# Kernel tuning notes

Hardware: AMD Instinct MI355X
Metric: run time of the kernel (lower is better)

The kernel has to match this reference:

```python
import jax, jax.numpy as jnp
import numpy as np

EPS = 1e-6

def _phi(x):
    # elu_feature_map: elu(x) + 1 (positive feature map)
    return jax.nn.elu(x) + 1.0

def setup_inputs() -> dict:
    key = jax.random.key(0)
    ks = jax.random.split(key, 6)
    N, L, S, H, E, D = 4, 2048, 2048, 16, 64, 64
    return {
        "queries1": jax.random.normal(ks[0], (N, L, H, E), jnp.float32),
        "keys1": jax.random.normal(ks[1], (N, S, H, E), jnp.float32),
        "values1": jax.random.normal(ks[2], (N, S, H, D), jnp.float32),
        "queries2": jax.random.normal(ks[3], (N, L, H, E), jnp.float32),
        "keys2": jax.random.normal(ks[4], (N, S, H, E), jnp.float32),
        "values2": jax.random.normal(ks[5], (N, S, H, D), jnp.float32),
        "key_lengths1": jnp.ones((N, S), jnp.float32),
        "key_lengths2": jnp.ones((N, S), jnp.float32),
    }

def _linear_cross(Q, K_other, V_other):
    # Q: (N,L,H,E) featurized queries; K_other: (N,S,H,E) featurized+masked keys
    # KV: (N,H,D,E) ; 'nshd,nshm->nhmd'
    KV = jnp.einsum('nshd,nshm->nhmd', K_other, V_other)
    Ksum = K_other.sum(axis=1)                      # (N,H,E)
    Z = 1.0 / (jnp.einsum('nlhd,nhd->nlh', Q, Ksum) + EPS)
    # 'nlhd,nhmd,nlh->nlhm'
    return jnp.einsum('nlhd,nhmd->nlhm', Q, KV) * Z[..., None]

def reference(queries1, keys1, values1, queries2, keys2, values2,
              key_lengths1, key_lengths2):
    Q1 = _phi(queries1)
    K1 = _phi(keys1) * key_lengths1[:, :, None, None]
    Q2 = _phi(queries2)
    K2 = _phi(keys2) * key_lengths2[:, :, None, None]
    V1 = _linear_cross(Q1, K2, values2)  # stream1 queries attend to stream2 keys/values
    V2 = _linear_cross(Q2, K1, values1)  # stream2 queries attend to stream1 keys/values
    return (V1, V2)
```

## Files before the change

kernel.cpp:

```cpp
#include <hip/hip_runtime.h>

#define NB 4
#define LL 2048
#define SS 2048
#define HH 16
#define EE 64
#define DD 64

#define KVTOT (2*NB*HH*4096)
#define WSFLOATS (KVTOT + 2*NB*HH*64)

typedef short short8 __attribute__((ext_vector_type(8)));
typedef float floatx4 __attribute__((ext_vector_type(4)));

__device__ inline float phi(float x) { return x > 0.f ? x + 1.f : __expf(x); }

__device__ inline unsigned int f2bf(float f) {
    unsigned int x = __float_as_uint(f);
    return (x + 0x7FFFu + ((x >> 16) & 1u)) >> 16;
}
__device__ inline void split_pack(float a, float b, unsigned int &hp, unsigned int &lp) {
    const unsigned int ha = f2bf(a), hb = f2bf(b);
    const float ra = a - __uint_as_float(ha << 16);
    const float rb = b - __uint_as_float(hb << 16);
    hp = (ha & 0xFFFFu) | (hb << 16);
    lp = (f2bf(ra) & 0xFFFFu) | (f2bf(rb) << 16);
}

__global__ __launch_bounds__(256) void kv_kernel(
    const float* __restrict__ k1, const float* __restrict__ v1,
    const float* __restrict__ k2, const float* __restrict__ v2,
    const float* __restrict__ kl1, const float* __restrict__ kl2,
    float* __restrict__ ws)
{
    const int b = blockIdx.x;
    const int chunk = b & 7;
    const int h = (b >> 3) & 15;
    const int n = (b >> 7) & 3;
    const int st = (b >> 9) & 1;
    const float* K  = st ? k1 : k2;
    const float* V  = st ? v1 : v2;
    const float* KL = st ? kl1 : kl2;

    __shared__ __align__(16) unsigned short KtH[64][72];
    __shared__ __align__(16) unsigned short KtL[64][72];
    __shared__ __align__(16) unsigned short VtH[64][72];
    __shared__ __align__(16) unsigned short VtL[64][72];

    const int t = threadIdx.x;
    const int lane = t & 63;
    const int w = t >> 6;
    const int d4 = t & 15;
    const int sp = t >> 4;
    const int c = lane & 15;
    const int q = lane >> 4;

    float ksum[4] = {0.f, 0.f, 0.f, 0.f};
    floatx4 acc[4];
#pragma unroll
    for (int i = 0; i < 4; i++) acc[i] = (floatx4){0.f, 0.f, 0.f, 0.f};

    float4 cur[8]; float curl[4];
    {
        const int sbase = chunk * 256;
#pragma unroll
        for (int i = 0; i < 2; ++i) {
            const int sl = 2 * sp + 32 * i;
            const size_t off = ((size_t)((size_t)n * SS + sbase + sl) * HH + h) * EE + 4 * d4;
            cur[4 * i + 0] = *(const float4*)&K[off];
            cur[4 * i + 1] = *(const float4*)&K[off + HH * EE];
            cur[4 * i + 2] = *(const float4*)&V[off];
            cur[4 * i + 3] = *(const float4*)&V[off + HH * EE];
            curl[2 * i + 0] = KL[(size_t)n * SS + sbase + sl];
            curl[2 * i + 1] = KL[(size_t)n * SS + sbase + sl + 1];
        }
    }

    for (int g = 0; g < 4; ++g) {
        float4 nxt[8]; float nxtl[4];
        if (g < 3) {
            const int sbase = chunk * 256 + (g + 1) * 64;
#pragma unroll
            for (int i = 0; i < 2; ++i) {
                const int sl = 2 * sp + 32 * i;
                const size_t off = ((size_t)((size_t)n * SS + sbase + sl) * HH + h) * EE + 4 * d4;
                nxt[4 * i + 0] = *(const float4*)&K[off];
                nxt[4 * i + 1] = *(const float4*)&K[off + HH * EE];
                nxt[4 * i + 2] = *(const float4*)&V[off];
                nxt[4 * i + 3] = *(const float4*)&V[off + HH * EE];
                nxtl[2 * i + 0] = KL[(size_t)n * SS + sbase + sl];
                nxtl[2 * i + 1] = KL[(size_t)n * SS + sbase + sl + 1];
            }
        }
        if (g) __syncthreads();
#pragma unroll
        for (int i = 0; i < 2; ++i) {
            const int sl = 2 * sp + 32 * i;
            const float4 ka = cur[4 * i + 0], kb = cur[4 * i + 1];
            const float4 va = cur[4 * i + 2], vb = cur[4 * i + 3];
            const float l0 = curl[2 * i + 0], l1 = curl[2 * i + 1];
            const float a0 = phi(ka.x) * l0, a1 = phi(ka.y) * l0;
            const float a2 = phi(ka.z) * l0, a3 = phi(ka.w) * l0;
            const float b0 = phi(kb.x) * l1, b1 = phi(kb.y) * l1;
            const float b2 = phi(kb.z) * l1, b3 = phi(kb.w) * l1;
            ksum[0] += a0 + b0; ksum[1] += a1 + b1;
            ksum[2] += a2 + b2; ksum[3] += a3 + b3;
            unsigned int hp, lp;
            split_pack(a0, b0, hp, lp);
            *(unsigned int*)&KtH[4 * d4 + 0][sl] = hp; *(unsigned int*)&KtL[4 * d4 + 0][sl] = lp;
            split_pack(a1, b1, hp, lp);
            *(unsigned int*)&KtH[4 * d4 + 1][sl] = hp; *(unsigned int*)&KtL[4 * d4 + 1][sl] = lp;
            split_pack(a2, b2, hp, lp);
            *(unsigned int*)&KtH[4 * d4 + 2][sl] = hp; *(unsigned int*)&KtL[4 * d4 + 2][sl] = lp;
            split_pack(a3, b3, hp, lp);
            *(unsigned int*)&KtH[4 * d4 + 3][sl] = hp; *(unsigned int*)&KtL[4 * d4 + 3][sl] = lp;
            split_pack(va.x, vb.x, hp, lp);
            *(unsigned int*)&VtH[4 * d4 + 0][sl] = hp; *(unsigned int*)&VtL[4 * d4 + 0][sl] = lp;
            split_pack(va.y, vb.y, hp, lp);
            *(unsigned int*)&VtH[4 * d4 + 1][sl] = hp; *(unsigned int*)&VtL[4 * d4 + 1][sl] = lp;
            split_pack(va.z, vb.z, hp, lp);
            *(unsigned int*)&VtH[4 * d4 + 2][sl] = hp; *(unsigned int*)&VtL[4 * d4 + 2][sl] = lp;
            split_pack(va.w, vb.w, hp, lp);
            *(unsigned int*)&VtH[4 * d4 + 3][sl] = hp; *(unsigned int*)&VtL[4 * d4 + 3][sl] = lp;
        }
        __syncthreads();
#pragma unroll
        for (int ks = 0; ks < 2; ++ks) {
            const short8 aH = *(const short8*)&VtH[16 * w + c][32 * ks + 8 * q];
            const short8 aL = *(const short8*)&VtL[16 * w + c][32 * ks + 8 * q];
#pragma unroll
            for (int dt = 0; dt < 4; ++dt) {
                const short8 bH = *(const short8*)&KtH[16 * dt + c][32 * ks + 8 * q];
                const short8 bL = *(const short8*)&KtL[16 * dt + c][32 * ks + 8 * q];
                acc[dt] = __builtin_amdgcn_mfma_f32_16x16x32_bf16(aH, bH, acc[dt], 0, 0, 0);
                acc[dt] = __builtin_amdgcn_mfma_f32_16x16x32_bf16(aH, bL, acc[dt], 0, 0, 0);
                acc[dt] = __builtin_amdgcn_mfma_f32_16x16x32_bf16(aL, bH, acc[dt], 0, 0, 0);
            }
        }
        if (g < 3) {
#pragma unroll
            for (int i = 0; i < 8; ++i) cur[i] = nxt[i];
#pragma unroll
            for (int i = 0; i < 4; ++i) curl[i] = nxtl[i];
        }
    }

    const size_t kvbase = ((size_t)((st * NB + n) * HH + h)) * 4096;
#pragma unroll
    for (int dt = 0; dt < 4; ++dt)
#pragma unroll
        for (int r = 0; r < 4; ++r)
            atomicAdd(&ws[kvbase + (size_t)(16 * w + 4 * q + r) * 64 + 16 * dt + c],
                      acc[dt][r]);

    float (*scr)[64] = (float(*)[64])VtL;
    __syncthreads();
    scr[sp][4 * d4 + 0] = ksum[0];
    scr[sp][4 * d4 + 1] = ksum[1];
    scr[sp][4 * d4 + 2] = ksum[2];
    scr[sp][4 * d4 + 3] = ksum[3];
    __syncthreads();
    if (t < 64) {
        float s = 0.f;
#pragma unroll
        for (int i = 0; i < 16; ++i) s += scr[i][t];
        atomicAdd(&ws[KVTOT + ((size_t)(st * NB + n) * HH + h) * 64 + t], s);
    }
}

static __device__ __forceinline__ float lt_body(
    const float4 qa0, const float4 qb0, const float4 qa1, const float4 qb1,
    const float* Ksp,
    const unsigned short (*BH)[72], const unsigned short (*BL)[72],
    const int c, const int q, floatx4* acc)
{
    float z = 0.f;
#pragma unroll
    for (int ks = 0; ks < 2; ++ks) {
        const float4 qa = ks ? qa1 : qa0;
        const float4 qb = ks ? qb1 : qb0;
        const int co = 32 * ks + 8 * q;
        const float p[8] = {phi(qa.x), phi(qa.y), phi(qa.z), phi(qa.w),
                            phi(qb.x), phi(qb.y), phi(qb.z), phi(qb.w)};
        z += p[0] * Ksp[co + 0] + p[1] * Ksp[co + 1]
           + p[2] * Ksp[co + 2] + p[3] * Ksp[co + 3]
           + p[4] * Ksp[co + 4] + p[5] * Ksp[co + 5]
           + p[6] * Ksp[co + 6] + p[7] * Ksp[co + 7];
        short8 aH, aL;
#pragma unroll
        for (int j = 0; j < 8; ++j) {
            const unsigned int hb = f2bf(p[j]);
            aH[j] = (short)hb;
            aL[j] = (short)f2bf(p[j] - __uint_as_float(hb << 16));
        }
#pragma unroll
        for (int mt = 0; mt < 4; ++mt) {
            const short8 bH = *(const short8*)&BH[16 * mt + c][co];
            const short8 bL = *(const short8*)&BL[16 * mt + c][co];
            acc[mt] = __builtin_amdgcn_mfma_f32_16x16x32_bf16(aH, bH, acc[mt], 0, 0, 0);
            acc[mt] = __builtin_amdgcn_mfma_f32_16x16x32_bf16(aH, bL, acc[mt], 0, 0, 0);
            acc[mt] = __builtin_amdgcn_mfma_f32_16x16x32_bf16(aL, bH, acc[mt], 0, 0, 0);
        }
    }
    return z;
}

__global__ __launch_bounds__(256) void out_kernel(
    const float* __restrict__ q1, const float* __restrict__ q2,
    const float* __restrict__ ws, float* __restrict__ out)
{
    const int b = blockIdx.x;
    const int lc = b & 15;
    const int h = (b >> 4) & 15;
    const int n = (b >> 8) & 3;
    const int st = (b >> 10) & 1;
    const float* Q = st ? q2 : q1;
    float* O = out + (size_t)st * ((size_t)NB * LL * HH * DD);

    __shared__ __align__(16) unsigned short BtH[64][72];
    __shared__ __align__(16) unsigned short BtL[64][72];
    __shared__ float Ks[64];

    const int t = threadIdx.x;
    const int lane = t & 63;
    const int w = t >> 6;
    const int c = lane & 15;
    const int q = lane >> 4;
    const size_t kvbase = ((size_t)((st * NB + n) * HH + h)) * 4096;
    const int lbase = lc * 128;

    const float* qr0 = &Q[((size_t)((size_t)n * LL + lbase + 32 * w + c) * HH + h) * EE];
    const int d0q = 8 * q;
    const float4 p00 = *(const float4*)&qr0[d0q];
    const float4 p01 = *(const float4*)&qr0[d0q + 4];
    const float4 p02 = *(const float4*)&qr0[d0q + 32];
    const float4 p03 = *(const float4*)&qr0[d0q + 36];

    {
        const int m = t >> 2;
        const int dbase = (t & 3) * 16;
#pragma unroll
        for (int i = 0; i < 4; ++i) {
            const int d0 = dbase + 4 * i;
            const float4 kv = *(const float4*)&ws[kvbase + (size_t)m * 64 + d0];
            unsigned int hp, lp;
            split_pack(kv.x, kv.y, hp, lp);
            *(unsigned int*)&BtH[m][d0]     = hp; *(unsigned int*)&BtL[m][d0]     = lp;
            split_pack(kv.z, kv.w, hp, lp);
            *(unsigned int*)&BtH[m][d0 + 2] = hp; *(unsigned int*)&BtL[m][d0 + 2] = lp;
        }
    }
    if (t < 64) Ks[t] = ws[KVTOT + ((size_t)(st * NB + n) * HH + h) * 64 + t];
    __syncthreads();

    floatx4 acc[8];
#pragma unroll
    for (int i = 0; i < 8; ++i) acc[i] = (floatx4){0.f, 0.f, 0.f, 0.f};

    float z0 = lt_body(p00, p01, p02, p03, Ks, BtH, BtL, c, q, acc);

    const float* qr1 = qr0 + (size_t)16 * HH * EE;
    const float4 p10 = *(const float4*)&qr1[d0q];
    const float4 p11 = *(const float4*)&qr1[d0q + 4];
    const float4 p12 = *(const float4*)&qr1[d0q + 32];
    const float4 p13 = *(const float4*)&qr1[d0q + 36];
    float z1 = lt_body(p10, p11, p12, p13, Ks, BtH, BtL, c, q, acc + 4);

    z0 += __shfl_xor(z0, 16); z0 += __shfl_xor(z0, 32);
    z1 += __shfl_xor(z1, 16); z1 += __shfl_xor(z1, 32);
    const float zi0 = 1.f / (z0 + 1e-6f);
    const float zi1 = 1.f / (z1 + 1e-6f);

#pragma unroll
    for (int lt = 0; lt < 2; ++lt) {
        const float zi = lt ? zi1 : zi0;
#pragma unroll
        for (int r = 0; r < 4; ++r) {
            const float zz = __shfl(zi, 4 * q + r);
            const int ll = 32 * w + 16 * lt + 4 * q + r;
            const size_t ro = ((size_t)((size_t)n * LL + lbase + ll) * HH + h) * DD;
#pragma unroll
            for (int mt = 0; mt < 4; ++mt)
                O[ro + 16 * mt + c] = acc[4 * lt + mt][r] * zz;
        }
    }
}

extern "C" void kernel_launch(void* const* d_in, const int* in_sizes, int n_in,
                              void* d_out, int out_size, void* d_ws, size_t ws_size,
                              hipStream_t stream) {
    const float* q1  = (const float*)d_in[0];
    const float* k1  = (const float*)d_in[1];
    const float* v1  = (const float*)d_in[2];
    const float* q2  = (const float*)d_in[3];
    const float* k2  = (const float*)d_in[4];
    const float* v2  = (const float*)d_in[5];
    const float* kl1 = (const float*)d_in[6];
    const float* kl2 = (const float*)d_in[7];
    float* ws = (float*)d_ws;
    float* out = (float*)d_out;

    hipMemsetAsync(d_ws, 0, (size_t)WSFLOATS * sizeof(float), stream);
    kv_kernel<<<dim3(1024), dim3(256), 0, stream>>>(k1, v1, k2, v2, kl1, kl2, ws);
    out_kernel<<<dim3(2048), dim3(256), 0, stream>>>(q1, q2, ws, out);
}
```

Before: 240.8 us.

## Replace KV atomics and memset with per-chunk partials and XOR-swizzled LDS

The KV kernel now writes per-chunk partial KV and Ksum results to separate workspace slots with plain stores, replacing atomicAdd. This removes the memset launch that zeroed the workspace. The out kernel sums the 8 chunk partials while loading KV, which adds 8x global reads per block across 2048 blocks. The LDS tiles also drop the 72-element padding in favour of an XOR swizzle to avoid bank conflicts.

Result: slower. 276.4 us (+14.8%).

```diff
diff --git a/kernel.cpp b/kernel.cpp
--- a/kernel.cpp
+++ b/kernel.cpp
@@ -7,8 +7,10 @@
 #define EE 64
 #define DD 64
 
-#define KVTOT (2*NB*HH*4096)
-#define WSFLOATS (KVTOT + 2*NB*HH*64)
+#define NHEAD (2*NB*HH)
+#define NCHUNK 8
+#define KVP ((size_t)NHEAD*NCHUNK*4096)
+#define WSFLOATS (KVP + (size_t)NHEAD*NCHUNK*64)
 
 typedef short short8 __attribute__((ext_vector_type(8)));
 typedef float floatx4 __attribute__((ext_vector_type(4)));
@@ -25,6 +27,10 @@
     const float rb = b - __uint_as_float(hb << 16);
     hp = (ha & 0xFFFFu) | (hb << 16);
     lp = (f2bf(ra) & 0xFFFFu) | (f2bf(rb) << 16);
+}
+
+__device__ inline int swz(int row, int col) {
+    return ((((col >> 3) ^ ((row >> 2) ^ row)) & 7) << 3) | (col & 7);
 }
 
 __global__ __launch_bounds__(256) void kv_kernel(
@@ -42,10 +48,10 @@
     const float* V  = st ? v1 : v2;
     const float* KL = st ? kl1 : kl2;
 
-    __shared__ __align__(16) unsigned short KtH[64][72];
-    __shared__ __align__(16) unsigned short KtL[64][72];
-    __shared__ __align__(16) unsigned short VtH[64][72];
-    __shared__ __align__(16) unsigned short VtL[64][72];
+    __shared__ __align__(16) unsigned short KtH[64][64];
+    __shared__ __align__(16) unsigned short KtL[64][64];
+    __shared__ __align__(16) unsigned short VtH[64][64];
+    __shared__ __align__(16) unsigned short VtL[64][64];
 
     const int t = threadIdx.x;
     const int lane = t & 63;
@@ -106,32 +112,39 @@
             ksum[0] += a0 + b0; ksum[1] += a1 + b1;
             ksum[2] += a2 + b2; ksum[3] += a3 + b3;
             unsigned int hp, lp;
+            const int r0 = 4 * d4;
+            const int s0 = swz(r0 + 0, sl), s1 = swz(r0 + 1, sl);
+            const int s2 = swz(r0 + 2, sl), s3 = swz(r0 + 3, sl);
             split_pack(a0, b0, hp, lp);
-            *(unsigned int*)&KtH[4 * d4 + 0][sl] = hp; *(unsigned int*)&KtL[4 * d4 + 0][sl] = lp;
+            *(unsigned int*)&KtH[r0 + 0][s0] = hp; *(unsigned int*)&KtL[r0 + 0][s0] = lp;
             split_pack(a1, b1, hp, lp);
-            *(unsigned int*)&KtH[4 * d4 + 1][sl] = hp; *(unsigned int*)&KtL[4 * d4 + 1][sl] = lp;
+            *(unsigned int*)&KtH[r0 + 1][s1] = hp; *(unsigned int*)&KtL[r0 + 1][s1] = lp;
             split_pack(a2, b2, hp, lp);
-            *(unsigned int*)&KtH[4 * d4 + 2][sl] = hp; *(unsigned int*)&KtL[4 * d4 + 2][sl] = lp;
+            *(unsigned int*)&KtH[r0 + 2][s2] = hp; *(unsigned int*)&KtL[r0 + 2][s2] = lp;
             split_pack(a3, b3, hp, lp);
-            *(unsigned int*)&KtH[4 * d4 + 3][sl] = hp; *(unsigned int*)&KtL[4 * d4 + 3][sl] = lp;
+            *(unsigned int*)&KtH[r0 + 3][s3] = hp; *(unsigned int*)&KtL[r0 + 3][s3] = lp;
             split_pack(va.x, vb.x, hp, lp);
-            *(unsigned int*)&VtH[4 * d4 + 0][sl] = hp; *(unsigned int*)&VtL[4 * d4 + 0][sl] = lp;
+            *(unsigned int*)&VtH[r0 + 0][s0] = hp; *(unsigned int*)&VtL[r0 + 0][s0] = lp;
             split_pack(va.y, vb.y, hp, lp);
-            *(unsigned int*)&VtH[4 * d4 + 1][sl] = hp; *(unsigned int*)&VtL[4 * d4 + 1][sl] = lp;
+            *(unsigned int*)&VtH[r0 + 1][s1] = hp; *(unsigned int*)&VtL[r0 + 1][s1] = lp;
             split_pack(va.z, vb.z, hp, lp);
-            *(unsigned int*)&VtH[4 * d4 + 2][sl] = hp; *(unsigned int*)&VtL[4 * d4 + 2][sl] = lp;
+            *(unsigned int*)&VtH[r0 + 2][s2] = hp; *(unsigned int*)&VtL[r0 + 2][s2] = lp;
             split_pack(va.w, vb.w, hp, lp);
-            *(unsigned int*)&VtH[4 * d4 + 3][sl] = hp; *(unsigned int*)&VtL[4 * d4 + 3][sl] = lp;
+            *(unsigned int*)&VtH[r0 + 3][s3] = hp; *(unsigned int*)&VtL[r0 + 3][s3] = lp;
         }
         __syncthreads();
+        const int ra = 16 * w + c;
 #pragma unroll
         for (int ks = 0; ks < 2; ++ks) {
-            const short8 aH = *(const short8*)&VtH[16 * w + c][32 * ks + 8 * q];
-            const short8 aL = *(const short8*)&VtL[16 * w + c][32 * ks + 8 * q];
+            const int ca = swz(ra, 32 * ks + 8 * q);
+            const short8 aH = *(const short8*)&VtH[ra][ca];
+            const short8 aL = *(const short8*)&VtL[ra][ca];
 #pragma unroll
             for (int dt = 0; dt < 4; ++dt) {
-                const short8 bH = *(const short8*)&KtH[16 * dt + c][32 * ks + 8 * q];
-                const short8 bL = *(const short8*)&KtL[16 * dt + c][32 * ks + 8 * q];
+                const int rb = 16 * dt + c;
+                const int cb = swz(rb, 32 * ks + 8 * q);
+                const short8 bH = *(const short8*)&KtH[rb][cb];
+                const short8 bL = *(const short8*)&KtL[rb][cb];
                 acc[dt] = __builtin_amdgcn_mfma_f32_16x16x32_bf16(aH, bH, acc[dt], 0, 0, 0);
                 acc[dt] = __builtin_amdgcn_mfma_f32_16x16x32_bf16(aH, bL, acc[dt], 0, 0, 0);
                 acc[dt] = __builtin_amdgcn_mfma_f32_16x16x32_bf16(aL, bH, acc[dt], 0, 0, 0);
@@ -145,13 +158,13 @@
         }
     }
 
-    const size_t kvbase = ((size_t)((st * NB + n) * HH + h)) * 4096;
+    const int head = (st * NB + n) * HH + h;
+    const size_t kvbase = ((size_t)head * NCHUNK + chunk) * 4096;
 #pragma unroll
     for (int dt = 0; dt < 4; ++dt)
 #pragma unroll
         for (int r = 0; r < 4; ++r)
-            atomicAdd(&ws[kvbase + (size_t)(16 * w + 4 * q + r) * 64 + 16 * dt + c],
-                      acc[dt][r]);
+            ws[kvbase + (size_t)(16 * w + 4 * q + r) * 64 + 16 * dt + c] = acc[dt][r];
 
     float (*scr)[64] = (float(*)[64])VtL;
     __syncthreads();
@@ -164,7 +177,7 @@
         float s = 0.f;
 #pragma unroll
         for (int i = 0; i < 16; ++i) s += scr[i][t];
-        atomicAdd(&ws[KVTOT + ((size_t)(st * NB + n) * HH + h) * 64 + t], s);
+        ws[KVP + ((size_t)head * NCHUNK + chunk) * 64 + t] = s;
     }
 }
 
@@ -226,7 +239,8 @@
     const int w = t >> 6;
     const int c = lane & 15;
     const int q = lane >> 4;
-    const size_t kvbase = ((size_t)((st * NB + n) * HH + h)) * 4096;
+    const int head = (st * NB + n) * HH + h;
+    const size_t kvb8 = (size_t)head * NCHUNK * 4096;
     const int lbase = lc * 128;
 
     const float* qr0 = &Q[((size_t)((size_t)n * LL + lbase + 32 * w + c) * HH + h) * EE];
@@ -242,7 +256,13 @@
 #pragma unroll
         for (int i = 0; i < 4; ++i) {
             const int d0 = dbase + 4 * i;
-            const float4 kv = *(const float4*)&ws[kvbase + (size_t)m * 64 + d0];
+            const size_t eo = (size_t)m * 64 + d0;
+            float4 kv = *(const float4*)&ws[kvb8 + eo];
+#pragma unroll
+            for (int ch = 1; ch < NCHUNK; ++ch) {
+                const float4 p = *(const float4*)&ws[kvb8 + (size_t)ch * 4096 + eo];
+                kv.x += p.x; kv.y += p.y; kv.z += p.z; kv.w += p.w;
+            }
             unsigned int hp, lp;
             split_pack(kv.x, kv.y, hp, lp);
             *(unsigned int*)&BtH[m][d0]     = hp; *(unsigned int*)&BtL[m][d0]     = lp;
@@ -250,7 +270,13 @@
             *(unsigned int*)&BtH[m][d0 + 2] = hp; *(unsigned int*)&BtL[m][d0 + 2] = lp;
         }
     }
-    if (t < 64) Ks[t] = ws[KVTOT + ((size_t)(st * NB + n) * HH + h) * 64 + t];
+    if (t < 64) {
+        float s = 0.f;
+#pragma unroll
+        for (int ch = 0; ch < NCHUNK; ++ch)
+            s += ws[KVP + ((size_t)head * NCHUNK + ch) * 64 + t];
+        Ks[t] = s;
+    }
     __syncthreads();
 
     floatx4 acc[8];
@@ -300,7 +326,6 @@
     float* ws = (float*)d_ws;
     float* out = (float*)d_out;
 
-    hipMemsetAsync(d_ws, 0, (size_t)WSFLOATS * sizeof(float), stream);
     kv_kernel<<<dim3(1024), dim3(256), 0, stream>>>(k1, v1, k2, v2, kl1, kl2, ws);
     out_kernel<<<dim3(2048), dim3(256), 0, stream>>>(q1, q2, ws, out);
 }
```
